# Kernel tuning notes

Hardware: AMD Instinct MI355X
Metric: run time of the kernel (lower is better)

## Reference

```python
import jax, jax.numpy as jnp
import numpy as np

H = 18  # hidden/input size hardcoded in the module
B, T = 1024, 1024

def _uniform(key, shape, scale):
    return jax.random.uniform(key, shape, jnp.float32, -scale, scale)

def setup_inputs() -> dict:
    key = jax.random.key(0)
    ks = jax.random.split(key, 12)
    s = 1.0 / np.sqrt(H)
    x = jax.random.normal(ks[0], (B, T, H), dtype=jnp.float32)
    return {
        "x": x,
        "gru_Wih": _uniform(ks[1], (3 * H, H), s),
        "gru_Whh": _uniform(ks[2], (3 * H, H), s),
        "gru_bih": _uniform(ks[3], (3 * H,), s),
        "gru_bhh": _uniform(ks[4], (3 * H,), s),
        "lstm_Wih": _uniform(ks[5], (4 * H, H), s),
        "lstm_Whh": _uniform(ks[6], (4 * H, H), s),
        "lstm_bih": _uniform(ks[7], (4 * H,), s),
        "lstm_bhh": _uniform(ks[8], (4 * H,), s),
        "fc_W": _uniform(ks[9], (1, H), s),
        "fc_b": _uniform(ks[10], (1,), s),
    }

def _gru(x, Wih, Whh, bih, bhh):
    # x: [B, T, H]. Precompute input contributions for all timesteps.
    xi = jnp.einsum("bth,gh->btg", x, Wih) + bih  # [B, T, 3H]
    xi_t = jnp.transpose(xi, (1, 0, 2))            # [T, B, 3H]
    h0 = jnp.zeros((x.shape[0], H), x.dtype)

    def step(h, xt):
        hh = h @ Whh.T + bhh                        # [B, 3H]
        xr, xz, xn = jnp.split(xt, 3, axis=-1)
        hr, hz, hn = jnp.split(hh, 3, axis=-1)
        r = jax.nn.sigmoid(xr + hr)
        z = jax.nn.sigmoid(xz + hz)
        n = jnp.tanh(xn + r * hn)
        h_new = (1.0 - z) * n + z * h
        return h_new, h_new

    _, hs = jax.lax.scan(step, h0, xi_t)
    return jnp.transpose(hs, (1, 0, 2))             # [B, T, H]

def _lstm(x, Wih, Whh, bih, bhh):
    xi = jnp.einsum("bth,gh->btg", x, Wih) + bih   # [B, T, 4H]
    xi_t = jnp.transpose(xi, (1, 0, 2))
    h0 = jnp.zeros((x.shape[0], H), x.dtype)
    c0 = jnp.zeros((x.shape[0], H), x.dtype)

    def step(carry, xt):
        h, c = carry
        g = xt + h @ Whh.T + bhh                    # [B, 4H]
        i, f, gg, o = jnp.split(g, 4, axis=-1)      # PyTorch gate order i,f,g,o
        i = jax.nn.sigmoid(i)
        f = jax.nn.sigmoid(f)
        gg = jnp.tanh(gg)
        o = jax.nn.sigmoid(o)
        c_new = f * c + i * gg
        h_new = o * jnp.tanh(c_new)
        return (h_new, c_new), h_new

    _, hs = jax.lax.scan(step, (h0, c0), xi_t)
    return jnp.transpose(hs, (1, 0, 2))

def reference(x, gru_Wih, gru_Whh, gru_bih, gru_bhh,
              lstm_Wih, lstm_Whh, lstm_bih, lstm_bhh, fc_W, fc_b):
    g = _gru(x, gru_Wih, gru_Whh, gru_bih, gru_bhh)
    l = _lstm(g, lstm_Wih, lstm_Whh, lstm_bih, lstm_bhh)
    return jnp.einsum("bth,oh->bto", l, fc_W) + fc_b  # [B, T, 1]
```

## Files before the change

kernel.cpp:

```cpp
#include <hip/hip_runtime.h>
#include <cstdint>
#include <cstddef>
#include <math.h>

#define Hh 18
#define Tt 1024
#define CHUNK 16
#define NCH (Tt / CHUNK)
#define XP 20

#define LC 1.44269504088896340736f

__device__ __forceinline__ float sigm_(float u) {
    return __fdividef(1.f, 1.f + exp2f(-LC * u));
}
__device__ __forceinline__ float tanh_(float u) {
    return fmaf(-2.f, __fdividef(1.f, 1.f + exp2f((2.f * LC) * u)), 1.f);
}
__device__ __forceinline__ void ld18_(float* d, const float* s) {
    *(float4*)&d[0]  = *(const float4*)&s[0];
    *(float4*)&d[4]  = *(const float4*)&s[4];
    *(float4*)&d[8]  = *(const float4*)&s[8];
    *(float4*)&d[12] = *(const float4*)&s[12];
    d[16] = s[16]; d[17] = s[17];
}
__device__ __forceinline__ float dot18_(const float* v, const float* w, float bias) {
    float a0 = bias, a1 = 0.f;
    #pragma unroll
    for (int k = 0; k < Hh; k += 2) {
        a0 = fmaf(w[k],     v[k],     a0);
        a1 = fmaf(w[k + 1], v[k + 1], a1);
    }
    return a0 + a1;
}

__global__ __launch_bounds__(128, 2) void rnn_fused2(
    const float* __restrict__ x,
    const float* __restrict__ gWih, const float* __restrict__ gWhh,
    const float* __restrict__ gbih, const float* __restrict__ gbhh,
    const float* __restrict__ lWih, const float* __restrict__ lWhh,
    const float* __restrict__ lbih, const float* __restrict__ lbhh,
    const float* __restrict__ fcW, const float* __restrict__ fcb,
    float* __restrict__ out)
{
    const int tid  = threadIdx.x;
    const int w    = tid >> 6;
    const int lane = tid & 63;
    const int b    = blockIdx.x;

    __shared__ __align__(16) float xs[2][CHUNK * XP];
    __shared__ __align__(16) float gbuf[2][XP];
    __shared__ __align__(16) float hlb[XP];
    __shared__ __align__(16) float xlb[2][80];

    float wA[Hh], wB[Hh], wE[Hh], wF[Hh];
    float b0, b1, b2 = 0.f, b3 = 0.f;
    if (w == 0) {
        const int rg = (lane < 54) ? lane : 0;
        #pragma unroll
        for (int k = 0; k < Hh; k++) {
            wA[k] = gWih[rg * Hh + k];
            wB[k] = gWhh[rg * Hh + k];
            wE[k] = lWih[lane * Hh + k];
            wF[k] = (lane < 8) ? lWih[(64 + lane) * Hh + k] : 0.f;
        }
        b0 = gbih[rg]; b1 = gbhh[rg];
        b2 = lbih[lane]; b3 = (lane < 8) ? lbih[64 + lane] : 0.f;
    } else {
        const int rs = (lane < 8) ? (64 + lane) : 64;
        #pragma unroll
        for (int k = 0; k < Hh; k++) {
            wA[k] = lWhh[lane * Hh + k];
            wB[k] = lWhh[rs * Hh + k];
            wE[k] = 0.f; wF[k] = 0.f;
        }
        b0 = lbhh[lane]; b1 = lbhh[rs];
    }

    const int i1 = (lane + 18) & 63;
    const int i2 = (lane + 36) & 63;
    const int i3 = (w == 0) ? ((lane - 36) & 63) : ((lane + 54) & 63);
    const int i4 = (lane - 10) & 63;

    const bool  isg = (w == 1) && (lane >= 36) && (lane < 54);
    const float kl  = isg ? (2.f * LC) : LC;
    const float Aa  = isg ? 2.f : 1.f;
    const float Bb  = isg ? -1.f : 0.f;

    const float fcw  = (w == 1 && lane < Hh) ? fcW[lane] : 0.f;
    const float fcbv = fcb[0];

    const float* xb   = x   + (size_t)b * (Tt * Hh);
    float*       outp = out + (size_t)b * Tt;

    if (w == 0 && lane < Hh) { gbuf[0][lane] = 0.f; gbuf[1][lane] = 0.f; }
    if (w == 1 && lane < Hh) { hlb[lane] = 0.f; }

    float p0 = 0, p1 = 0, p2 = 0, p3 = 0, p4 = 0;
    if (w == 0) {
        p0 = xb[lane]; p1 = xb[lane + 64]; p2 = xb[lane + 128]; p3 = xb[lane + 192];
        if (lane < 32) p4 = xb[lane + 256];
        int j;
        j = lane;       xs[0][(j / Hh) * XP + (j % Hh)] = p0;
        j = lane + 64;  xs[0][(j / Hh) * XP + (j % Hh)] = p1;
        j = lane + 128; xs[0][(j / Hh) * XP + (j % Hh)] = p2;
        j = lane + 192; xs[0][(j / Hh) * XP + (j % Hh)] = p3;
        if (lane < 32) { j = lane + 256; xs[0][(j / Hh) * XP + (j % Hh)] = p4; }
    }
    __syncthreads();

    float myh = 0.f, myc = 0.f;
    float o0 = 0, o1 = 0, o2 = 0, o3 = 0;

    for (int c = 0; c < NCH; c++) {
        const int cb = c & 1;
        if (w == 0 && c + 1 < NCH) {
            const float* xn = xb + (c + 1) * (CHUNK * Hh);
            p0 = xn[lane]; p1 = xn[lane + 64]; p2 = xn[lane + 128]; p3 = xn[lane + 192];
            if (lane < 32) p4 = xn[lane + 256];
        }
        #pragma unroll 2
        for (int s = 0; s < CHUNK; s++) {
            const int it = c * CHUNK + s;
            if (w == 0) {
                float xv[Hh], hv[Hh], gv[Hh];
                ld18_(xv, &xs[cb][s * XP]);
                ld18_(hv, gbuf[(it + 1) & 1]);
                const float xa = dot18_(xv, wA, b0);
                const float ha = dot18_(hv, wB, b1);
                const float sg = sigm_(xa + ha);
                const float rv = __shfl(sg, i3, 64);
                const float un = fmaf(rv, ha, xa);
                const float tn = tanh_(un);
                const float zz = __shfl(sg, i1, 64);
                const float nn = __shfl(tn, i2, 64);
                const float hnew = fmaf(zz, myh - nn, nn);
                if (lane < Hh) { myh = hnew; gbuf[it & 1][lane] = hnew; }
                __builtin_amdgcn_wave_barrier();
                ld18_(gv, gbuf[it & 1]);
                const float xl  = dot18_(gv, wE, b2);
                const float xl2 = dot18_(gv, wF, b3);
                xlb[it & 1][lane] = xl;
                if (lane < 8) xlb[it & 1][64 + lane] = xl2;
            } else if (it > 0) {
                const int u = it - 1;
                float hv[Hh];
                ld18_(hv, hlb);
                const float hla = dot18_(hv, wA, b0);
                const float hl2 = dot18_(hv, wB, b1);
                const float xl  = xlb[u & 1][lane];
                const float xl2 = xlb[u & 1][64 + (lane & 7)];
                const float ul  = xl + hla;
                const float a3  = fmaf(Aa, __fdividef(1.f, 1.f + exp2f(-kl * ul)), Bb);
                const float a4  = sigm_(xl2 + hl2);
                const float ff  = __shfl(a3, i1, 64);
                const float gg  = __shfl(a3, i2, 64);
                const float oa  = __shfl(a3, i3, 64);
                const float ob  = __shfl(a4, i4, 64);
                const float oo  = (lane < 10) ? oa : ob;
                const float cn  = ff * myc + a3 * gg;
                if (lane < Hh) myc = cn;
                const float tc  = tanh_(cn);
                const float hlv = oo * tc;
                if (lane < Hh) hlb[lane] = hlv;
                __builtin_amdgcn_wave_barrier();
                float fv = fcw * hlv;
                fv += __shfl_xor(fv, 1, 64);
                fv += __shfl_xor(fv, 2, 64);
                fv += __shfl_xor(fv, 4, 64);
                fv += __shfl_xor(fv, 8, 64);
                fv += __shfl_xor(fv, 16, 64);
                const float ov = fv + fcbv;
                const int sm = u & 3;
                if (sm == 0) o0 = ov; else if (sm == 1) o1 = ov; else if (sm == 2) o2 = ov; else o3 = ov;
                if (sm == 3 && lane == 0) {
                    float4 vv; vv.x = o0; vv.y = o1; vv.z = o2; vv.w = o3;
                    *reinterpret_cast<float4*>(outp + u - 3) = vv;
                }
            }
            __syncthreads();
        }
        if (w == 0 && c + 1 < NCH) {
            const int nb = cb ^ 1;
            int j;
            j = lane;       xs[nb][(j / Hh) * XP + (j % Hh)] = p0;
            j = lane + 64;  xs[nb][(j / Hh) * XP + (j % Hh)] = p1;
            j = lane + 128; xs[nb][(j / Hh) * XP + (j % Hh)] = p2;
            j = lane + 192; xs[nb][(j / Hh) * XP + (j % Hh)] = p3;
            if (lane < 32) { j = lane + 256; xs[nb][(j / Hh) * XP + (j % Hh)] = p4; }
        }
    }

    if (w == 1) {
        const int u = Tt - 1;
        float hv[Hh];
        ld18_(hv, hlb);
        const float hla = dot18_(hv, wA, b0);
        const float hl2 = dot18_(hv, wB, b1);
        const float xl  = xlb[u & 1][lane];
        const float xl2 = xlb[u & 1][64 + (lane & 7)];
        const float ul  = xl + hla;
        const float a3  = fmaf(Aa, __fdividef(1.f, 1.f + exp2f(-kl * ul)), Bb);
        const float a4  = sigm_(xl2 + hl2);
        const float ff  = __shfl(a3, i1, 64);
        const float gg  = __shfl(a3, i2, 64);
        const float oa  = __shfl(a3, i3, 64);
        const float ob  = __shfl(a4, i4, 64);
        const float oo  = (lane < 10) ? oa : ob;
        const float cn  = ff * myc + a3 * gg;
        const float tc  = tanh_(cn);
        const float hlv = oo * tc;
        float fv = fcw * hlv;
        fv += __shfl_xor(fv, 1, 64);
        fv += __shfl_xor(fv, 2, 64);
        fv += __shfl_xor(fv, 4, 64);
        fv += __shfl_xor(fv, 8, 64);
        fv += __shfl_xor(fv, 16, 64);
        const float ov = fv + fcbv;
        o3 = ov;
        if (lane == 0) {
            float4 vv; vv.x = o0; vv.y = o1; vv.z = o2; vv.w = o3;
            *reinterpret_cast<float4*>(outp + u - 3) = vv;
        }
    }
}

extern "C" void kernel_launch(void* const* d_in, const int* in_sizes, int n_in,
                              void* d_out, int out_size, void* d_ws, size_t ws_size,
                              hipStream_t stream)
{
    const float* xx   = (const float*)d_in[0];
    const float* gWih = (const float*)d_in[1];
    const float* gWhh = (const float*)d_in[2];
    const float* gbih = (const float*)d_in[3];
    const float* gbhh = (const float*)d_in[4];
    const float* lWih = (const float*)d_in[5];
    const float* lWhh = (const float*)d_in[6];
    const float* lbih = (const float*)d_in[7];
    const float* lbhh = (const float*)d_in[8];
    const float* fcW  = (const float*)d_in[9];
    const float* fcb  = (const float*)d_in[10];
    float* outp = (float*)d_out;

    dim3 grid(1024), block(128);
    hipLaunchKernelGGL(rnn_fused2, grid, block, 0, stream,
                       xx, gWih, gWhh, gbih, gbhh,
                       lWih, lWhh, lbih, lbhh, fcW, fcb, outp);
}
```

Baseline: 642.2 us.

## Add third wave for GRU input projection and sync once per 8-step window

Splits work across three waves per block. A new wave loads x and computes the GRU input projections ahead of time into a ring buffer. The GRU wave handles the recurrence plus the LSTM input projection, and the LSTM wave lags by one 8-step window. Block-wide barriers drop from once per timestep to once per window, which takes the input-projection dot product off the GRU critical path. The cost is an extra wave of registers per block and a launch-bounds change to 192 threads.

```diff
diff --git a/kernel.cpp b/kernel.cpp
--- a/kernel.cpp
+++ b/kernel.cpp
@@ -5,9 +5,8 @@
 
 #define Hh 18
 #define Tt 1024
-#define CHUNK 16
-#define NCH (Tt / CHUNK)
-#define XP 20
+#define WSTEP 8
+#define NW (Tt / WSTEP)
 
 #define LC 1.44269504088896340736f
 
@@ -34,7 +33,7 @@
     return a0 + a1;
 }
 
-__global__ __launch_bounds__(128, 2) void rnn_fused2(
+__global__ __launch_bounds__(192, 3) void rnn_fused3(
     const float* __restrict__ x,
     const float* __restrict__ gWih, const float* __restrict__ gWhh,
     const float* __restrict__ gbih, const float* __restrict__ gbhh,
@@ -44,90 +43,112 @@
     float* __restrict__ out)
 {
     const int tid  = threadIdx.x;
-    const int w    = tid >> 6;
+    const int role = tid >> 6;
     const int lane = tid & 63;
     const int b    = blockIdx.x;
 
-    __shared__ __align__(16) float xs[2][CHUNK * XP];
-    __shared__ __align__(16) float gbuf[2][XP];
-    __shared__ __align__(16) float hlb[XP];
-    __shared__ __align__(16) float xlb[2][80];
-
-    float wA[Hh], wB[Hh], wE[Hh], wF[Hh];
-    float b0, b1, b2 = 0.f, b3 = 0.f;
-    if (w == 0) {
+    __shared__ __align__(16) float xab[16][64];
+    __shared__ __align__(16) float xlb[16][80];
+    __shared__ __align__(16) float xst[2][WSTEP][20];
+    __shared__ __align__(16) float gbuf[20];
+    __shared__ __align__(16) float hlb[20];
+
+    float wA[Hh], wB[Hh], wC[Hh];
+    float b0 = 0.f, b1 = 0.f, b2 = 0.f;
+    if (role == 0) {
         const int rg = (lane < 54) ? lane : 0;
         #pragma unroll
         for (int k = 0; k < Hh; k++) {
-            wA[k] = gWih[rg * Hh + k];
-            wB[k] = gWhh[rg * Hh + k];
-            wE[k] = lWih[lane * Hh + k];
-            wF[k] = (lane < 8) ? lWih[(64 + lane) * Hh + k] : 0.f;
-        }
-        b0 = gbih[rg]; b1 = gbhh[rg];
-        b2 = lbih[lane]; b3 = (lane < 8) ? lbih[64 + lane] : 0.f;
-    } else {
+            wA[k] = gWhh[rg * Hh + k];
+            wB[k] = lWih[lane * Hh + k];
+            wC[k] = (lane < 8) ? lWih[(64 + lane) * Hh + k] : 0.f;
+        }
+        b0 = gbhh[rg];
+        b1 = lbih[lane];
+        b2 = (lane < 8) ? lbih[64 + lane] : 0.f;
+    } else if (role == 1) {
         const int rs = (lane < 8) ? (64 + lane) : 64;
         #pragma unroll
         for (int k = 0; k < Hh; k++) {
             wA[k] = lWhh[lane * Hh + k];
             wB[k] = lWhh[rs * Hh + k];
-            wE[k] = 0.f; wF[k] = 0.f;
+            wC[k] = 0.f;
         }
         b0 = lbhh[lane]; b1 = lbhh[rs];
+    } else {
+        const int rg = (lane < 54) ? lane : 0;
+        #pragma unroll
+        for (int k = 0; k < Hh; k++) {
+            wA[k] = gWih[rg * Hh + k];
+            wB[k] = 0.f; wC[k] = 0.f;
+        }
+        b0 = gbih[rg];
     }
 
     const int i1 = (lane + 18) & 63;
     const int i2 = (lane + 36) & 63;
-    const int i3 = (w == 0) ? ((lane - 36) & 63) : ((lane + 54) & 63);
+    const int i3 = (role == 0) ? ((lane - 36) & 63) : ((lane + 54) & 63);
     const int i4 = (lane - 10) & 63;
 
-    const bool  isg = (w == 1) && (lane >= 36) && (lane < 54);
+    const bool  isg = (role == 1) && (lane >= 36) && (lane < 54);
     const float kl  = isg ? (2.f * LC) : LC;
     const float Aa  = isg ? 2.f : 1.f;
     const float Bb  = isg ? -1.f : 0.f;
 
-    const float fcw  = (w == 1 && lane < Hh) ? fcW[lane] : 0.f;
+    const float fcw  = (role == 1 && lane < Hh) ? fcW[lane] : 0.f;
     const float fcbv = fcb[0];
 
     const float* xb   = x   + (size_t)b * (Tt * Hh);
     float*       outp = out + (size_t)b * Tt;
 
-    if (w == 0 && lane < Hh) { gbuf[0][lane] = 0.f; gbuf[1][lane] = 0.f; }
-    if (w == 1 && lane < Hh) { hlb[lane] = 0.f; }
-
-    float p0 = 0, p1 = 0, p2 = 0, p3 = 0, p4 = 0;
-    if (w == 0) {
-        p0 = xb[lane]; p1 = xb[lane + 64]; p2 = xb[lane + 128]; p3 = xb[lane + 192];
-        if (lane < 32) p4 = xb[lane + 256];
-        int j;
-        j = lane;       xs[0][(j / Hh) * XP + (j % Hh)] = p0;
-        j = lane + 64;  xs[0][(j / Hh) * XP + (j % Hh)] = p1;
-        j = lane + 128; xs[0][(j / Hh) * XP + (j % Hh)] = p2;
-        j = lane + 192; xs[0][(j / Hh) * XP + (j % Hh)] = p3;
-        if (lane < 32) { j = lane + 256; xs[0][(j / Hh) * XP + (j % Hh)] = p4; }
-    }
-    __syncthreads();
-
     float myh = 0.f, myc = 0.f;
     float o0 = 0, o1 = 0, o2 = 0, o3 = 0;
-
-    for (int c = 0; c < NCH; c++) {
-        const int cb = c & 1;
-        if (w == 0 && c + 1 < NCH) {
-            const float* xn = xb + (c + 1) * (CHUNK * Hh);
-            p0 = xn[lane]; p1 = xn[lane + 64]; p2 = xn[lane + 128]; p3 = xn[lane + 192];
-            if (lane < 32) p4 = xn[lane + 256];
-        }
-        #pragma unroll 2
-        for (int s = 0; s < CHUNK; s++) {
-            const int it = c * CHUNK + s;
-            if (w == 0) {
-                float xv[Hh], hv[Hh], gv[Hh];
-                ld18_(xv, &xs[cb][s * XP]);
-                ld18_(hv, gbuf[(it + 1) & 1]);
-                const float xa = dot18_(xv, wA, b0);
-                const float ha = dot18_(hv, wB, b1);
+    float px0 = 0.f, px1 = 0.f, px2 = 0.f;
+
+    if (role == 0 && lane < Hh) gbuf[lane] = 0.f;
+    if (role == 1 && lane < Hh) hlb[lane]  = 0.f;
+    if (role == 2) {
+        px0 = xb[lane]; px1 = xb[64 + lane]; px2 = (lane < 16) ? xb[128 + lane] : 0.f;
+        { int j = lane;      xst[0][j / Hh][j % Hh] = px0;
+          j = 64 + lane;     xst[0][j / Hh][j % Hh] = px1;
+          if (lane < 16) { j = 128 + lane; xst[0][j / Hh][j % Hh] = px2; } }
+        #pragma unroll
+        for (int j = 0; j < WSTEP; j++) {
+            float xr[Hh]; ld18_(xr, &xst[0][j][0]);
+            xab[j][lane] = dot18_(xr, wA, b0);
+        }
+        const float* xw = xb + WSTEP * Hh;
+        px0 = xw[lane]; px1 = xw[64 + lane]; if (lane < 16) px2 = xw[128 + lane];
+    }
+
+    for (int w = 0; w <= NW; w++) {
+        __syncthreads();
+
+        if (role == 2 && w <= NW - 2) {
+            const int W = w + 1;
+            const int xbuf = W & 1;
+            { int j = lane;      xst[xbuf][j / Hh][j % Hh] = px0;
+              j = 64 + lane;     xst[xbuf][j / Hh][j % Hh] = px1;
+              if (lane < 16) { j = 128 + lane; xst[xbuf][j / Hh][j % Hh] = px2; } }
+            if (w + 2 <= NW - 1) {
+                const float* xw = xb + (size_t)(w + 2) * (WSTEP * Hh);
+                px0 = xw[lane]; px1 = xw[64 + lane]; if (lane < 16) px2 = xw[128 + lane];
+            }
+            #pragma unroll
+            for (int j = 0; j < WSTEP; j++) {
+                float xr[Hh]; ld18_(xr, &xst[xbuf][j][0]);
+                xab[(8 * W + j) & 15][lane] = dot18_(xr, wA, b0);
+            }
+        }
+
+        if (role == 0 && w <= NW - 1) {
+            #pragma unroll 4
+            for (int j = 0; j < WSTEP; j++) {
+                const int t = 8 * w + j;
+                float hv[Hh];
+                ld18_(hv, gbuf);
+                const float xa = xab[t & 15][lane];
+                const float ha = dot18_(hv, wA, b0);
                 const float sg = sigm_(xa + ha);
                 const float rv = __shfl(sg, i3, 64);
                 const float un = fmaf(rv, ha, xa);
@@ -135,21 +156,27 @@
                 const float zz = __shfl(sg, i1, 64);
                 const float nn = __shfl(tn, i2, 64);
                 const float hnew = fmaf(zz, myh - nn, nn);
-                if (lane < Hh) { myh = hnew; gbuf[it & 1][lane] = hnew; }
+                if (lane < Hh) { myh = hnew; gbuf[lane] = hnew; }
                 __builtin_amdgcn_wave_barrier();
-                ld18_(gv, gbuf[it & 1]);
-                const float xl  = dot18_(gv, wE, b2);
-                const float xl2 = dot18_(gv, wF, b3);
-                xlb[it & 1][lane] = xl;
-                if (lane < 8) xlb[it & 1][64 + lane] = xl2;
-            } else if (it > 0) {
-                const int u = it - 1;
+                float gv[Hh];
+                ld18_(gv, gbuf);
+                const float xl  = dot18_(gv, wB, b1);
+                const float xl2 = dot18_(gv, wC, b2);
+                xlb[t & 15][lane] = xl;
+                if (lane < 8) xlb[t & 15][64 + lane] = xl2;
+            }
+        }
+
+        if (role == 1 && w >= 1) {
+            #pragma unroll 4
+            for (int j = 0; j < WSTEP; j++) {
+                const int u = 8 * (w - 1) + j;
                 float hv[Hh];
                 ld18_(hv, hlb);
                 const float hla = dot18_(hv, wA, b0);
                 const float hl2 = dot18_(hv, wB, b1);
-                const float xl  = xlb[u & 1][lane];
-                const float xl2 = xlb[u & 1][64 + (lane & 7)];
+                const float xl  = xlb[u & 15][lane];
+                const float xl2 = xlb[u & 15][64 + (lane & 7)];
                 const float ul  = xl + hla;
                 const float a3  = fmaf(Aa, __fdividef(1.f, 1.f + exp2f(-kl * ul)), Bb);
                 const float a4  = sigm_(xl2 + hl2);
@@ -171,56 +198,13 @@
                 fv += __shfl_xor(fv, 8, 64);
                 fv += __shfl_xor(fv, 16, 64);
                 const float ov = fv + fcbv;
-                const int sm = u & 3;
+                const int sm = j & 3;
                 if (sm == 0) o0 = ov; else if (sm == 1) o1 = ov; else if (sm == 2) o2 = ov; else o3 = ov;
                 if (sm == 3 && lane == 0) {
                     float4 vv; vv.x = o0; vv.y = o1; vv.z = o2; vv.w = o3;
                     *reinterpret_cast<float4*>(outp + u - 3) = vv;
                 }
             }
-            __syncthreads();
-        }
-        if (w == 0 && c + 1 < NCH) {
-            const int nb = cb ^ 1;
-            int j;
-            j = lane;       xs[nb][(j / Hh) * XP + (j % Hh)] = p0;
-            j = lane + 64;  xs[nb][(j / Hh) * XP + (j % Hh)] = p1;
-            j = lane + 128; xs[nb][(j / Hh) * XP + (j % Hh)] = p2;
-            j = lane + 192; xs[nb][(j / Hh) * XP + (j % Hh)] = p3;
-            if (lane < 32) { j = lane + 256; xs[nb][(j / Hh) * XP + (j % Hh)] = p4; }
-        }
-    }
-
-    if (w == 1) {
-        const int u = Tt - 1;
-        float hv[Hh];
-        ld18_(hv, hlb);
-        const float hla = dot18_(hv, wA, b0);
-        const float hl2 = dot18_(hv, wB, b1);
-        const float xl  = xlb[u & 1][lane];
-        const float xl2 = xlb[u & 1][64 + (lane & 7)];
-        const float ul  = xl + hla;
-        const float a3  = fmaf(Aa, __fdividef(1.f, 1.f + exp2f(-kl * ul)), Bb);
-        const float a4  = sigm_(xl2 + hl2);
-        const float ff  = __shfl(a3, i1, 64);
-        const float gg  = __shfl(a3, i2, 64);
-        const float oa  = __shfl(a3, i3, 64);
-        const float ob  = __shfl(a4, i4, 64);
-        const float oo  = (lane < 10) ? oa : ob;
-        const float cn  = ff * myc + a3 * gg;
-        const float tc  = tanh_(cn);
-        const float hlv = oo * tc;
-        float fv = fcw * hlv;
-        fv += __shfl_xor(fv, 1, 64);
-        fv += __shfl_xor(fv, 2, 64);
-        fv += __shfl_xor(fv, 4, 64);
-        fv += __shfl_xor(fv, 8, 64);
-        fv += __shfl_xor(fv, 16, 64);
-        const float ov = fv + fcbv;
-        o3 = ov;
-        if (lane == 0) {
-            float4 vv; vv.x = o0; vv.y = o1; vv.z = o2; vv.w = o3;
-            *reinterpret_cast<float4*>(outp + u - 3) = vv;
         }
     }
 }
@@ -242,8 +226,8 @@
     const float* fcb  = (const float*)d_in[10];
     float* outp = (float*)d_out;
 
-    dim3 grid(1024), block(128);
-    hipLaunchKernelGGL(rnn_fused2, grid, block, 0, stream,
+    dim3 grid(1024), block(192);
+    hipLaunchKernelGGL(rnn_fused3, grid, block, 0, stream,
                        xx, gWih, gWhh, gbih, gbhh,
                        lWih, lWhh, lbih, lbhh, fcW, fcb, outp);
 }
```

After: 523.5 us. -18.5%, faster.
